# Optimization experiments

Measured on AMD Instinct MI355X. Metric: run time of the kernel, lower is better.

## Reference

```python
import jax, jax.numpy as jnp
import numpy as np

B, N, D = 16, 128, 128
NEG = jnp.float32(-9e15)
LRELU_SLOPE = 0.2
HOMO_EDGES = [1, 2, 3, 4]
HETE_EDGES = [1, 5, 6, 7, 8, 9, 10]


def _mlp_proj(x, w1, b1, w2, b2):
    # Linear(D,D) -> ReLU -> Linear(D,1)
    return jax.nn.relu(x @ w1 + b1) @ w2 + b2


def setup_inputs() -> dict:
    key = jax.random.key(0)
    ks = jax.random.split(key, 16)
    s = 0.05
    return {
        "hidden": jax.random.normal(ks[0], (B, N, D), dtype=jnp.float32),
        "adj": jax.random.randint(ks[1], (B, N, N), 0, 11),
        "node_type_mask": jax.random.randint(ks[2], (B, N), 0, 4),
        "W_Q": jax.random.normal(ks[3], (4, D, D), dtype=jnp.float32) * s,
        "W_K": jax.random.normal(ks[4], (4, D, D), dtype=jnp.float32) * s,
        "W_V": jax.random.normal(ks[5], (4, D, D), dtype=jnp.float32) * s,
        "a": jax.random.normal(ks[6], (4, D), dtype=jnp.float32) * s,  # a_params, squeezed [D,1]->[D]
        "p_w1": jax.random.normal(ks[7], (D, D), dtype=jnp.float32) * s,
        "p_b1": jnp.zeros((D,), jnp.float32),
        "p_w2": jax.random.normal(ks[8], (D, 1), dtype=jnp.float32) * s,
        "p_b2": jnp.zeros((1,), jnp.float32),
        "g_w1": jax.random.normal(ks[9], (D, D), dtype=jnp.float32) * s,
        "g_b1": jnp.zeros((D,), jnp.float32),
        "g_w2": jax.random.normal(ks[10], (D, 1), dtype=jnp.float32) * s,
        "g_b2": jnp.zeros((1,), jnp.float32),
    }


def _forward(hidden, adj, node_type_mask, W_Q, W_K, W_V, a,
             p_w1, p_b1, p_w2, p_b2, g_w1, g_b1, g_w2, g_b2):
    b, n, d = hidden.shape
    flat = hidden.reshape(-1, d)                      # [B*N, D]
    mask = node_type_mask.reshape(-1)                 # [B*N]

    # typed Q projection; nodes of type 0 stay zero (matches source)
    qh = jnp.zeros_like(flat)
    for t in range(1, 4):
        qh = jnp.where((mask == t)[:, None], flat @ W_Q[t], qh)
    q = qh.reshape(b, n, d)
    # NOTE: source bug preserved — key/value are copies of query
    k = q
    v = q

    lrelu = lambda x: jax.nn.leaky_relu(x, LRELU_SLOPE)

    # ---- homo attention on value_hidden ----
    a_input = v[:, :, None, :] * v[:, None, :, :]     # [B,N,N,D] pairwise product
    alpha = jnp.full((b, n, n), NEG, dtype=hidden.dtype)
    for r in HOMO_EDGES:
        e = lrelu(jnp.einsum('bijd,d->bij', a_input, a[r - 1]))
        alpha = jnp.where(adj == r, e, alpha)
    homo_w = jax.nn.softmax(alpha, axis=-1)
    homo_output = homo_w @ v                          # [B,N,D]

    # ---- hete attention ----
    scross = jnp.einsum('bqd,bkd->bqk', q, k)         # [B,N,N]
    global_a = jnp.tanh(scross)
    global_output = global_a @ v
    scores = jnp.full_like(scross, NEG)
    for r in HETE_EDGES:
        scores = jnp.where(adj == r, scross, scores)
    scores = lrelu(scores)
    hete_w = jax.nn.softmax(scores, axis=-1)
    hete_output = hete_w @ v                          # [B,N,D]

    # ---- gate fusion ----
    input_h = jnp.stack([homo_output, hete_output], axis=-2)   # [B,N,2,D]
    energy = _mlp_proj(input_h, p_w1, p_b1, p_w2, p_b2)        # [B,N,2,1]
    w = jax.nn.softmax(energy[..., 0], axis=-1)
    local_output = (input_h * w[..., None]).sum(axis=-2)       # [B,N,D]

    input_h2 = jnp.stack([local_output, global_output], axis=-2)
    energy2 = _mlp_proj(input_h2, g_w1, g_b1, g_w2, g_b2)
    w2 = jax.nn.softmax(energy2[..., 0], axis=-1)
    attention_output = (input_h2 * w2[..., None]).sum(axis=-2)
    return attention_output


def reference(hidden, adj, node_type_mask, W_Q, W_K, W_V, a,
              p_w1, p_b1, p_w2, p_b2, g_w1, g_b1, g_w2, g_b2):
    return _forward(hidden, adj, node_type_mask, W_Q, W_K, W_V, a,
                    p_w1, p_b1, p_w2, p_b2, g_w1, g_b1, g_w2, g_b2)
```

## Files before the change

kernel.cpp:

```cpp
#include <hip/hip_runtime.h>
#include <math.h>

#define BB 16
#define NN 128
#define DD 128
#define NEGV (-9e15f)
#define SLOPE 0.2f

__global__ __launch_bounds__(128) void hete_qproj(
    const float* __restrict__ hidden, const int* __restrict__ mask,
    const float* __restrict__ WQ, float* __restrict__ q)
{
    const int r = blockIdx.x;
    const int d = threadIdx.x;
    __shared__ float h[DD];
    h[d] = hidden[r * DD + d];
    __syncthreads();
    const int t = mask[r];
    if (t == 0) { q[r * DD + d] = 0.f; return; }
    const float* W = WQ + t * DD * DD;
    float acc = 0.f;
#pragma unroll 8
    for (int k = 0; k < DD; ++k)
        acc = fmaf(h[k], W[k * DD + d], acc);
    q[r * DD + d] = acc;
}

__global__ __launch_bounds__(256) void hete_fused(
    const float* __restrict__ q, const int* __restrict__ adj,
    const float* __restrict__ aparam,
    const float* __restrict__ p_w1, const float* __restrict__ p_b1,
    const float* __restrict__ p_w2, const float* __restrict__ p_b2,
    const float* __restrict__ g_w1, const float* __restrict__ g_b1,
    const float* __restrict__ g_w2, const float* __restrict__ g_b2,
    float* __restrict__ out)
{
    __shared__ float qs[NN][DD];
    __shared__ float a_s[4][132];
    __shared__ float wrow[2][3][NN];
    __shared__ float red[4][8];
    __shared__ float enr[8];
    __shared__ __align__(16) float ro[4][3][132];

    const int tid  = threadIdx.x;
    const int b    = blockIdx.x >> 5;
    const int chunk= blockIdx.x & 31;
    const int eh   = tid >> 7;
    const int j    = tid & 127;
    const int wv   = tid >> 6;
    const int lane = tid & 63;

    const float* qb = q + b * NN * DD;
    for (int it = 0; it < (NN * DD) / 256; ++it) {
        int idx = it * 256 + tid;
        int jj = idx >> 7, dd = idx & 127;
        qs[jj][dd ^ (jj & 31)] = qb[idx];
    }
    for (int it = 0; it < 2; ++it) {
        int idx = it * 256 + tid;
        a_s[idx >> 7][idx & 127] = aparam[idx];
    }
    __syncthreads();

    for (int rp = 0; rp < 2; ++rp) {
        const int rL = rp * 2 + eh;
        const int ri = chunk * 4 + rL;
        const int adjv = adj[(b * NN + ri) * NN + j];
        const bool inH = (adjv >= 1 && adjv <= 4);
        const bool inT = (adjv == 1) || (adjv >= 5);
        const int  rh  = inH ? (adjv - 1) : 0;
        const int  risw = ri & 31;

        float s = 0.f, hm = 0.f;
#pragma unroll 4
        for (int d = 0; d < DD; ++d) {
            float qi = qs[ri][d ^ risw];
            float qj = qs[j][d ^ (j & 31)];
            float p  = qi * qj;
            s += p;
            hm = fmaf(p, a_s[rh][d], hm);
        }

        float gw = tanhf(s);
        float aH = inH ? (hm > 0.f ? hm : SLOPE * hm) : NEGV;
        float sT = inT ? s : NEGV;
        sT = (sT > 0.f) ? sT : SLOPE * sT;

        float mH = aH, mT = sT;
        for (int off = 32; off; off >>= 1) {
            mH = fmaxf(mH, __shfl_xor(mH, off));
            mT = fmaxf(mT, __shfl_xor(mT, off));
        }
        if (lane == 0) { red[wv][0] = mH; red[wv][1] = mT; }
        __syncthreads();
        mH = fmaxf(red[eh * 2][0], red[eh * 2 + 1][0]);
        mT = fmaxf(red[eh * 2][1], red[eh * 2 + 1][1]);
        float eHv = expf(aH - mH);
        float eTv = expf(sT - mT);
        float sumH = eHv, sumT = eTv;
        for (int off = 32; off; off >>= 1) {
            sumH += __shfl_xor(sumH, off);
            sumT += __shfl_xor(sumT, off);
        }
        __syncthreads();
        if (lane == 0) { red[wv][0] = sumH; red[wv][1] = sumT; }
        __syncthreads();
        sumH = red[eh * 2][0] + red[eh * 2 + 1][0];
        sumT = red[eh * 2][1] + red[eh * 2 + 1][1];
        wrow[eh][0][j] = eHv / sumH;
        wrow[eh][1][j] = eTv / sumT;
        wrow[eh][2][j] = gw;
        __syncthreads();

        const int d = j;
        float accH = 0.f, accT = 0.f, accG = 0.f;
#pragma unroll 4
        for (int jj = 0; jj < NN; ++jj) {
            float qv = qs[jj][d ^ (jj & 31)];
            accH = fmaf(wrow[eh][0][jj], qv, accH);
            accT = fmaf(wrow[eh][1][jj], qv, accT);
            accG = fmaf(wrow[eh][2][jj], qv, accG);
        }
        ro[rL][0][d] = accH;
        ro[rL][1][d] = accT;
        ro[rL][2][d] = accG;
        __syncthreads();
    }

    const int u = j;
    {
        float a0 = 0.f, a1 = 0.f, a2 = 0.f, a3 = 0.f;
        for (int k = 0; k < DD; k += 4) {
            float w0 = p_w1[(k + 0) * DD + u];
            float w1 = p_w1[(k + 1) * DD + u];
            float w2 = p_w1[(k + 2) * DD + u];
            float w3 = p_w1[(k + 3) * DD + u];
            const float4 x0 = *reinterpret_cast<const float4*>(&ro[eh * 2 + 0][0][k]);
            const float4 x1 = *reinterpret_cast<const float4*>(&ro[eh * 2 + 0][1][k]);
            const float4 x2 = *reinterpret_cast<const float4*>(&ro[eh * 2 + 1][0][k]);
            const float4 x3 = *reinterpret_cast<const float4*>(&ro[eh * 2 + 1][1][k]);
            a0 = fmaf(x0.x, w0, fmaf(x0.y, w1, fmaf(x0.z, w2, fmaf(x0.w, w3, a0))));
            a1 = fmaf(x1.x, w0, fmaf(x1.y, w1, fmaf(x1.z, w2, fmaf(x1.w, w3, a1))));
            a2 = fmaf(x2.x, w0, fmaf(x2.y, w1, fmaf(x2.z, w2, fmaf(x2.w, w3, a2))));
            a3 = fmaf(x3.x, w0, fmaf(x3.y, w1, fmaf(x3.z, w2, fmaf(x3.w, w3, a3))));
        }
        float pb1 = p_b1[u], pw2 = p_w2[u];
        float c0 = fmaxf(a0 + pb1, 0.f) * pw2;
        float c1 = fmaxf(a1 + pb1, 0.f) * pw2;
        float c2 = fmaxf(a2 + pb1, 0.f) * pw2;
        float c3 = fmaxf(a3 + pb1, 0.f) * pw2;
        for (int off = 32; off; off >>= 1) {
            c0 += __shfl_xor(c0, off);
            c1 += __shfl_xor(c1, off);
            c2 += __shfl_xor(c2, off);
            c3 += __shfl_xor(c3, off);
        }
        if (lane == 0) { red[wv][0] = c0; red[wv][1] = c1; red[wv][2] = c2; red[wv][3] = c3; }
    }
    __syncthreads();
    if (tid < 8) {
        int half = tid >> 2;
        enr[tid] = red[half * 2][tid & 3] + red[half * 2 + 1][tid & 3] + p_b2[0];
    }
    __syncthreads();
#pragma unroll
    for (int rr = 0; rr < 2; ++rr) {
        int rL = eh * 2 + rr;
        float e0 = enr[rL * 2], e1 = enr[rL * 2 + 1];
        float m  = fmaxf(e0, e1);
        float x0 = expf(e0 - m), x1 = expf(e1 - m);
        float inv = 1.f / (x0 + x1);
        ro[rL][0][u] = (x0 * ro[rL][0][u] + x1 * ro[rL][1][u]) * inv;
    }
    __syncthreads();

    {
        float a0 = 0.f, a1 = 0.f, a2 = 0.f, a3 = 0.f;
        for (int k = 0; k < DD; k += 4) {
            float w0 = g_w1[(k + 0) * DD + u];
            float w1 = g_w1[(k + 1) * DD + u];
            float w2 = g_w1[(k + 2) * DD + u];
            float w3 = g_w1[(k + 3) * DD + u];
            const float4 x0 = *reinterpret_cast<const float4*>(&ro[eh * 2 + 0][0][k]);
            const float4 x1 = *reinterpret_cast<const float4*>(&ro[eh * 2 + 0][2][k]);
            const float4 x2 = *reinterpret_cast<const float4*>(&ro[eh * 2 + 1][0][k]);
            const float4 x3 = *reinterpret_cast<const float4*>(&ro[eh * 2 + 1][2][k]);
            a0 = fmaf(x0.x, w0, fmaf(x0.y, w1, fmaf(x0.z, w2, fmaf(x0.w, w3, a0))));
            a1 = fmaf(x1.x, w0, fmaf(x1.y, w1, fmaf(x1.z, w2, fmaf(x1.w, w3, a1))));
            a2 = fmaf(x2.x, w0, fmaf(x2.y, w1, fmaf(x2.z, w2, fmaf(x2.w, w3, a2))));
            a3 = fmaf(x3.x, w0, fmaf(x3.y, w1, fmaf(x3.z, w2, fmaf(x3.w, w3, a3))));
        }
        float gb1 = g_b1[u], gw2 = g_w2[u];
        float c0 = fmaxf(a0 + gb1, 0.f) * gw2;
        float c1 = fmaxf(a1 + gb1, 0.f) * gw2;
        float c2 = fmaxf(a2 + gb1, 0.f) * gw2;
        float c3 = fmaxf(a3 + gb1, 0.f) * gw2;
        for (int off = 32; off; off >>= 1) {
            c0 += __shfl_xor(c0, off);
            c1 += __shfl_xor(c1, off);
            c2 += __shfl_xor(c2, off);
            c3 += __shfl_xor(c3, off);
        }
        __syncthreads();
        if (lane == 0) { red[wv][0] = c0; red[wv][1] = c1; red[wv][2] = c2; red[wv][3] = c3; }
    }
    __syncthreads();
    if (tid < 8) {
        int half = tid >> 2;
        enr[tid] = red[half * 2][tid & 3] + red[half * 2 + 1][tid & 3] + g_b2[0];
    }
    __syncthreads();
#pragma unroll
    for (int rr = 0; rr < 2; ++rr) {
        int rL = eh * 2 + rr;
        float e0 = enr[rL * 2], e1 = enr[rL * 2 + 1];
        float m  = fmaxf(e0, e1);
        float x0 = expf(e0 - m), x1 = expf(e1 - m);
        float inv = 1.f / (x0 + x1);
        float val = (x0 * ro[rL][0][u] + x1 * ro[rL][2][u]) * inv;
        out[(b * NN + chunk * 4 + rL) * DD + u] = val;
    }
}

extern "C" void kernel_launch(void* const* d_in, const int* in_sizes, int n_in,
                              void* d_out, int out_size, void* d_ws, size_t ws_size,
                              hipStream_t stream) {
    const float* hidden = (const float*)d_in[0];
    const int*   adj    = (const int*)d_in[1];
    const int*   mask   = (const int*)d_in[2];
    const float* W_Q    = (const float*)d_in[3];
    const float* aparam = (const float*)d_in[6];
    const float* p_w1   = (const float*)d_in[7];
    const float* p_b1   = (const float*)d_in[8];
    const float* p_w2   = (const float*)d_in[9];
    const float* p_b2   = (const float*)d_in[10];
    const float* g_w1   = (const float*)d_in[11];
    const float* g_b1   = (const float*)d_in[12];
    const float* g_w2   = (const float*)d_in[13];
    const float* g_b2   = (const float*)d_in[14];
    float* out = (float*)d_out;
    float* qws = (float*)d_ws;

    hete_qproj<<<BB * NN, 128, 0, stream>>>(hidden, mask, W_Q, qws);
    hete_fused<<<BB * 32, 256, 0, stream>>>(qws, adj, aparam,
                                            p_w1, p_b1, p_w2, p_b2,
                                            g_w1, g_b1, g_w2, g_b2, out);
}
```

Baseline: 120.2 us.

## Rewrite fused attention kernel with bf16 split-precision MFMA and larger row tiles

Replaces the scalar FP32 pairwise-score, homo-attention and gate-MLP loops with MFMA 16x16x32 bf16 instructions, using a hi/lo bf16 split to approximate FP32 accuracy. Each block now handles 8 rows with 512 threads, precomputes q*a for the four homo edge types, and caches adj in LDS. A separate transpose kernel prepares the gate weights for the MFMA layout. The weighted-sum stage reads V as bf16-hi only, and tanh/exp become fast approximations, which lowers precision.

```diff
diff --git a/kernel.cpp b/kernel.cpp
--- a/kernel.cpp
+++ b/kernel.cpp
@@ -6,6 +6,23 @@
 #define DD 128
 #define NEGV (-9e15f)
 #define SLOPE 0.2f
+
+typedef __attribute__((ext_vector_type(8))) short bf16x8;
+typedef __attribute__((ext_vector_type(4))) float f32x4;
+
+__device__ __forceinline__ float fast_tanh(float x) {
+    float e = __expf(2.f * x);
+    return 1.f - 2.f / (e + 1.f);
+}
+__device__ __forceinline__ float bf2f(short s) {
+    union { unsigned u; float f; } v; v.u = ((unsigned)(unsigned short)s) << 16; return v.f;
+}
+__device__ __forceinline__ short f2bf(float f) {
+    union { float f; unsigned u; } v; v.f = f;
+    unsigned r = v.u + 0x7FFF + ((v.u >> 16) & 1);
+    return (short)(r >> 16);
+}
+__device__ __forceinline__ int swz(int row, int oct) { return row * 256 + ((oct ^ (row & 7)) << 4); }
 
 __global__ __launch_bounds__(128) void hete_qproj(
     const float* __restrict__ hidden, const int* __restrict__ mask,
@@ -26,199 +43,319 @@
     q[r * DD + d] = acc;
 }
 
-__global__ __launch_bounds__(256) void hete_fused(
+__global__ __launch_bounds__(256) void transpose2(
+    const float* __restrict__ A, const float* __restrict__ B,
+    float* __restrict__ AT, float* __restrict__ BT)
+{
+    __shared__ float t[16][17];
+    const int mat = blockIdx.x >> 6, tile = blockIdx.x & 63;
+    const int tr = tile >> 3, tc = tile & 7;
+    const float* S = mat ? B : A;
+    float* D = mat ? BT : AT;
+    const int r = threadIdx.x >> 4, c = threadIdx.x & 15;
+    t[r][c] = S[(tr * 16 + r) * DD + tc * 16 + c];
+    __syncthreads();
+    D[(tc * 16 + r) * DD + tr * 16 + c] = t[c][r];
+}
+
+constexpr int QH_   = 0;
+constexpr int QL_   = 32768;
+constexpr int QCHH_ = 65536;
+constexpr int QCHL_ = 69632;
+constexpr int QA_   = 73728;
+constexpr int ADJ_  = 81920;
+constexpr int WMAT_ = 86016;
+constexpr int RO_   = 102400;
+constexpr int RED_  = 114688;
+constexpr int GRED_ = 115712;
+constexpr int ENR_  = 116224;
+constexpr int SMEM_ = 116288;
+
+#define MFMA(a, b, c) __builtin_amdgcn_mfma_f32_16x16x32_bf16((a), (b), (c), 0, 0, 0)
+
+__global__ __launch_bounds__(512) void hete_fused(
     const float* __restrict__ q, const int* __restrict__ adj,
     const float* __restrict__ aparam,
-    const float* __restrict__ p_w1, const float* __restrict__ p_b1,
-    const float* __restrict__ p_w2, const float* __restrict__ p_b2,
-    const float* __restrict__ g_w1, const float* __restrict__ g_b1,
-    const float* __restrict__ g_w2, const float* __restrict__ g_b2,
+    const float* __restrict__ w1t, const float* __restrict__ g1t,
+    const float* __restrict__ p_b1, const float* __restrict__ p_w2, const float* __restrict__ p_b2,
+    const float* __restrict__ g_b1, const float* __restrict__ g_w2, const float* __restrict__ g_b2,
     float* __restrict__ out)
 {
-    __shared__ float qs[NN][DD];
-    __shared__ float a_s[4][132];
-    __shared__ float wrow[2][3][NN];
-    __shared__ float red[4][8];
-    __shared__ float enr[8];
-    __shared__ __align__(16) float ro[4][3][132];
-
-    const int tid  = threadIdx.x;
-    const int b    = blockIdx.x >> 5;
-    const int chunk= blockIdx.x & 31;
-    const int eh   = tid >> 7;
-    const int j    = tid & 127;
-    const int wv   = tid >> 6;
-    const int lane = tid & 63;
-
+    __shared__ __align__(16) char smem[SMEM_];
+    const int tid   = threadIdx.x;
+    const int b     = blockIdx.x >> 4;
+    const int chunk = blockIdx.x & 15;
+    const int wv    = tid >> 6;
+    const int lane  = tid & 63;
+    const int l15   = lane & 15;
+    const int l4    = lane >> 4;
+    const int i7    = lane & 7;
     const float* qb = q + b * NN * DD;
-    for (int it = 0; it < (NN * DD) / 256; ++it) {
-        int idx = it * 256 + tid;
-        int jj = idx >> 7, dd = idx & 127;
-        qs[jj][dd ^ (jj & 31)] = qb[idx];
-    }
-    for (int it = 0; it < 2; ++it) {
-        int idx = it * 256 + tid;
-        a_s[idx >> 7][idx & 127] = aparam[idx];
+
+#pragma unroll
+    for (int it = 0; it < 4; ++it) {
+        int oct = it * 512 + tid;
+        int row = oct >> 4, o = oct & 15;
+        const f32x4* src = (const f32x4*)(qb + row * DD + o * 8);
+        f32x4 x0 = src[0], x1 = src[1];
+        float xs[8] = {x0.x, x0.y, x0.z, x0.w, x1.x, x1.y, x1.z, x1.w};
+        bf16x8 h, l;
+#pragma unroll
+        for (int e = 0; e < 8; ++e) { short hb = f2bf(xs[e]); h[e] = hb; l[e] = f2bf(xs[e] - bf2f(hb)); }
+        *(bf16x8*)(smem + QH_ + swz(row, o)) = h;
+        *(bf16x8*)(smem + QL_ + swz(row, o)) = l;
+    }
+    if (tid < 256) {
+        int n = tid >> 4, o = tid & 15;
+        bf16x8 h = {0,0,0,0,0,0,0,0}, l = {0,0,0,0,0,0,0,0};
+        if (n < 8) {
+            const f32x4* src = (const f32x4*)(qb + (chunk * 8 + n) * DD + o * 8);
+            f32x4 x0 = src[0], x1 = src[1];
+            float xs[8] = {x0.x, x0.y, x0.z, x0.w, x1.x, x1.y, x1.z, x1.w};
+#pragma unroll
+            for (int e = 0; e < 8; ++e) { short hb = f2bf(xs[e]); h[e] = hb; l[e] = f2bf(xs[e] - bf2f(hb)); }
+        }
+        *(bf16x8*)(smem + QCHH_ + swz(n, o)) = h;
+        *(bf16x8*)(smem + QCHL_ + swz(n, o)) = l;
+    }
+    {
+        int nr = tid >> 4, o = tid & 15;
+        int t = nr >> 3, r8 = nr & 7;
+        const f32x4* sq = (const f32x4*)(qb + (chunk * 8 + r8) * DD + o * 8);
+        const f32x4* sa = (const f32x4*)(aparam + t * DD + o * 8);
+        f32x4 q0 = sq[0], q1 = sq[1], a0 = sa[0], a1 = sa[1];
+        bf16x8 v;
+        v[0] = f2bf(q0.x * a0.x); v[1] = f2bf(q0.y * a0.y);
+        v[2] = f2bf(q0.z * a0.z); v[3] = f2bf(q0.w * a0.w);
+        v[4] = f2bf(q1.x * a1.x); v[5] = f2bf(q1.y * a1.y);
+        v[6] = f2bf(q1.z * a1.z); v[7] = f2bf(q1.w * a1.w);
+        *(bf16x8*)(smem + QA_ + swz(nr, o)) = v;
+    }
+    if (tid < 256) {
+        const int4* s = (const int4*)(adj + (b * NN + chunk * 8) * NN);
+        ((int4*)(smem + ADJ_))[tid] = s[tid];
     }
     __syncthreads();
 
-    for (int rp = 0; rp < 2; ++rp) {
-        const int rL = rp * 2 + eh;
-        const int ri = chunk * 4 + rL;
-        const int adjv = adj[(b * NN + ri) * NN + j];
-        const bool inH = (adjv >= 1 && adjv <= 4);
-        const bool inT = (adjv == 1) || (adjv >= 5);
-        const int  rh  = inH ? (adjv - 1) : 0;
-        const int  risw = ri & 31;
-
-        float s = 0.f, hm = 0.f;
+    f32x4 accS  = {0.f, 0.f, 0.f, 0.f};
+    f32x4 accH0 = {0.f, 0.f, 0.f, 0.f};
+    f32x4 accH1 = {0.f, 0.f, 0.f, 0.f};
+    {
+        const int arow = wv * 16 + l15;
+#pragma unroll
+        for (int ks = 0; ks < 4; ++ks) {
+            int o = ks * 4 + l4;
+            bf16x8 Ah = *(const bf16x8*)(smem + QH_  + swz(arow, o));
+            bf16x8 Al = *(const bf16x8*)(smem + QL_  + swz(arow, o));
+            bf16x8 Bh = *(const bf16x8*)(smem + QCHH_ + swz(l15, o));
+            bf16x8 Bl = *(const bf16x8*)(smem + QCHL_ + swz(l15, o));
+            bf16x8 Q0 = *(const bf16x8*)(smem + QA_ + swz(l15, o));
+            bf16x8 Q1 = *(const bf16x8*)(smem + QA_ + swz(16 + l15, o));
+            accS  = MFMA(Ah, Bh, accS);
+            accS  = MFMA(Ah, Bl, accS);
+            accS  = MFMA(Al, Bh, accS);
+            accH0 = MFMA(Ah, Q0, accH0);
+            accH0 = MFMA(Al, Q0, accH0);
+            accH1 = MFMA(Ah, Q1, accH1);
+            accH1 = MFMA(Al, Q1, accH1);
+        }
+    }
+
+    {
+        f32x4 pH0, pH1;
+#pragma unroll
+        for (int r = 0; r < 4; ++r) {
+            pH0[r] = __shfl_xor(accH0[r], 8);
+            pH1[r] = __shfl_xor(accH1[r], 8);
+        }
+        const bool low = (l15 < 8);
+        const int* adjl = (const int*)(smem + ADJ_);
+        float aHv[4], sTv[4], gwv[4];
+#pragma unroll
+        for (int r = 0; r < 4; ++r) {
+            int j = wv * 16 + l4 * 4 + r;
+            int adjv = adjl[i7 * NN + j];
+            float s = accS[r];
+            float hm = (adjv <= 2) ? ((adjv == 1) ? accH0[r] : pH0[r])
+                                   : ((adjv == 3) ? accH1[r] : pH1[r]);
+            bool inH = (adjv >= 1) & (adjv <= 4);
+            bool inT = (adjv == 1) | (adjv >= 5);
+            float aH = inH ? (hm > 0.f ? hm : SLOPE * hm) : NEGV;
+            float sT = inT ? s : NEGV; sT = sT > 0.f ? sT : SLOPE * sT;
+            aHv[r] = aH; sTv[r] = sT; gwv[r] = fast_tanh(s);
+        }
+        float mH = fmaxf(fmaxf(aHv[0], aHv[1]), fmaxf(aHv[2], aHv[3]));
+        float mT = fmaxf(fmaxf(sTv[0], sTv[1]), fmaxf(sTv[2], sTv[3]));
+        mH = fmaxf(mH, __shfl_xor(mH, 16)); mH = fmaxf(mH, __shfl_xor(mH, 32));
+        mT = fmaxf(mT, __shfl_xor(mT, 16)); mT = fmaxf(mT, __shfl_xor(mT, 32));
+        float* red = (float*)(smem + RED_);
+        if (low && l4 == 0) { red[(wv * 8 + l15) * 4 + 0] = mH; red[(wv * 8 + l15) * 4 + 1] = mT; }
+        __syncthreads();
+        float gmH = NEGV, gmT = NEGV;
+#pragma unroll
+        for (int w = 0; w < 8; ++w) {
+            gmH = fmaxf(gmH, red[(w * 8 + i7) * 4 + 0]);
+            gmT = fmaxf(gmT, red[(w * 8 + i7) * 4 + 1]);
+        }
+        float eH[4], eT[4], pHs = 0.f, pTs = 0.f;
+#pragma unroll
+        for (int r = 0; r < 4; ++r) {
+            eH[r] = __expf(aHv[r] - gmH); pHs += eH[r];
+            eT[r] = __expf(sTv[r] - gmT); pTs += eT[r];
+        }
+        pHs += __shfl_xor(pHs, 16); pHs += __shfl_xor(pHs, 32);
+        pTs += __shfl_xor(pTs, 16); pTs += __shfl_xor(pTs, 32);
+        if (low && l4 == 0) { red[(wv * 8 + l15) * 4 + 2] = pHs; red[(wv * 8 + l15) * 4 + 3] = pTs; }
+        __syncthreads();
+        float sH = 0.f, sT2 = 0.f;
+#pragma unroll
+        for (int w = 0; w < 8; ++w) {
+            sH  += red[(w * 8 + i7) * 4 + 2];
+            sT2 += red[(w * 8 + i7) * 4 + 3];
+        }
+        float invH = 1.f / sH, invT = 1.f / sT2;
+        if (low) {
+            float4* wm = (float4*)(smem + WMAT_);
+#pragma unroll
+            for (int r = 0; r < 4; ++r) {
+                int j = wv * 16 + l4 * 4 + r;
+                wm[l15 * NN + j] = make_float4(eH[r] * invH, eT[r] * invT, gwv[r], 0.f);
+            }
+        }
+        __syncthreads();
+    }
+
+    {
+        float a0[8] = {0,0,0,0,0,0,0,0}, a1[8] = {0,0,0,0,0,0,0,0}, a2[8] = {0,0,0,0,0,0,0,0};
+        const float4* wm = (const float4*)(smem + WMAT_) + wv * NN;
 #pragma unroll 4
-        for (int d = 0; d < DD; ++d) {
-            float qi = qs[ri][d ^ risw];
-            float qj = qs[j][d ^ (j & 31)];
-            float p  = qi * qj;
-            s += p;
-            hm = fmaf(p, a_s[rh][d], hm);
-        }
-
-        float gw = tanhf(s);
-        float aH = inH ? (hm > 0.f ? hm : SLOPE * hm) : NEGV;
-        float sT = inT ? s : NEGV;
-        sT = (sT > 0.f) ? sT : SLOPE * sT;
-
-        float mH = aH, mT = sT;
-        for (int off = 32; off; off >>= 1) {
-            mH = fmaxf(mH, __shfl_xor(mH, off));
-            mT = fmaxf(mT, __shfl_xor(mT, off));
-        }
-        if (lane == 0) { red[wv][0] = mH; red[wv][1] = mT; }
-        __syncthreads();
-        mH = fmaxf(red[eh * 2][0], red[eh * 2 + 1][0]);
-        mT = fmaxf(red[eh * 2][1], red[eh * 2 + 1][1]);
-        float eHv = expf(aH - mH);
-        float eTv = expf(sT - mT);
-        float sumH = eHv, sumT = eTv;
-        for (int off = 32; off; off >>= 1) {
-            sumH += __shfl_xor(sumH, off);
-            sumT += __shfl_xor(sumT, off);
-        }
-        __syncthreads();
-        if (lane == 0) { red[wv][0] = sumH; red[wv][1] = sumT; }
-        __syncthreads();
-        sumH = red[eh * 2][0] + red[eh * 2 + 1][0];
-        sumT = red[eh * 2][1] + red[eh * 2 + 1][1];
-        wrow[eh][0][j] = eHv / sumH;
-        wrow[eh][1][j] = eTv / sumT;
-        wrow[eh][2][j] = gw;
-        __syncthreads();
-
-        const int d = j;
-        float accH = 0.f, accT = 0.f, accG = 0.f;
-#pragma unroll 4
-        for (int jj = 0; jj < NN; ++jj) {
-            float qv = qs[jj][d ^ (jj & 31)];
-            accH = fmaf(wrow[eh][0][jj], qv, accH);
-            accT = fmaf(wrow[eh][1][jj], qv, accT);
-            accG = fmaf(wrow[eh][2][jj], qv, accG);
-        }
-        ro[rL][0][d] = accH;
-        ro[rL][1][d] = accT;
-        ro[rL][2][d] = accG;
-        __syncthreads();
-    }
-
-    const int u = j;
-    {
-        float a0 = 0.f, a1 = 0.f, a2 = 0.f, a3 = 0.f;
-        for (int k = 0; k < DD; k += 4) {
-            float w0 = p_w1[(k + 0) * DD + u];
-            float w1 = p_w1[(k + 1) * DD + u];
-            float w2 = p_w1[(k + 2) * DD + u];
-            float w3 = p_w1[(k + 3) * DD + u];
-            const float4 x0 = *reinterpret_cast<const float4*>(&ro[eh * 2 + 0][0][k]);
-            const float4 x1 = *reinterpret_cast<const float4*>(&ro[eh * 2 + 0][1][k]);
-            const float4 x2 = *reinterpret_cast<const float4*>(&ro[eh * 2 + 1][0][k]);
-            const float4 x3 = *reinterpret_cast<const float4*>(&ro[eh * 2 + 1][1][k]);
-            a0 = fmaf(x0.x, w0, fmaf(x0.y, w1, fmaf(x0.z, w2, fmaf(x0.w, w3, a0))));
-            a1 = fmaf(x1.x, w0, fmaf(x1.y, w1, fmaf(x1.z, w2, fmaf(x1.w, w3, a1))));
-            a2 = fmaf(x2.x, w0, fmaf(x2.y, w1, fmaf(x2.z, w2, fmaf(x2.w, w3, a2))));
-            a3 = fmaf(x3.x, w0, fmaf(x3.y, w1, fmaf(x3.z, w2, fmaf(x3.w, w3, a3))));
-        }
-        float pb1 = p_b1[u], pw2 = p_w2[u];
-        float c0 = fmaxf(a0 + pb1, 0.f) * pw2;
-        float c1 = fmaxf(a1 + pb1, 0.f) * pw2;
-        float c2 = fmaxf(a2 + pb1, 0.f) * pw2;
-        float c3 = fmaxf(a3 + pb1, 0.f) * pw2;
-        for (int off = 32; off; off >>= 1) {
-            c0 += __shfl_xor(c0, off);
-            c1 += __shfl_xor(c1, off);
-            c2 += __shfl_xor(c2, off);
-            c3 += __shfl_xor(c3, off);
-        }
-        if (lane == 0) { red[wv][0] = c0; red[wv][1] = c1; red[wv][2] = c2; red[wv][3] = c3; }
-    }
-    __syncthreads();
-    if (tid < 8) {
-        int half = tid >> 2;
-        enr[tid] = red[half * 2][tid & 3] + red[half * 2 + 1][tid & 3] + p_b2[0];
-    }
-    __syncthreads();
-#pragma unroll
-    for (int rr = 0; rr < 2; ++rr) {
-        int rL = eh * 2 + rr;
-        float e0 = enr[rL * 2], e1 = enr[rL * 2 + 1];
-        float m  = fmaxf(e0, e1);
-        float x0 = expf(e0 - m), x1 = expf(e1 - m);
-        float inv = 1.f / (x0 + x1);
-        ro[rL][0][u] = (x0 * ro[rL][0][u] + x1 * ro[rL][1][u]) * inv;
-    }
-    __syncthreads();
-
-    {
-        float a0 = 0.f, a1 = 0.f, a2 = 0.f, a3 = 0.f;
-        for (int k = 0; k < DD; k += 4) {
-            float w0 = g_w1[(k + 0) * DD + u];
-            float w1 = g_w1[(k + 1) * DD + u];
-            float w2 = g_w1[(k + 2) * DD + u];
-            float w3 = g_w1[(k + 3) * DD + u];
-            const float4 x0 = *reinterpret_cast<const float4*>(&ro[eh * 2 + 0][0][k]);
-            const float4 x1 = *reinterpret_cast<const float4*>(&ro[eh * 2 + 0][2][k]);
-            const float4 x2 = *reinterpret_cast<const float4*>(&ro[eh * 2 + 1][0][k]);
-            const float4 x3 = *reinterpret_cast<const float4*>(&ro[eh * 2 + 1][2][k]);
-            a0 = fmaf(x0.x, w0, fmaf(x0.y, w1, fmaf(x0.z, w2, fmaf(x0.w, w3, a0))));
-            a1 = fmaf(x1.x, w0, fmaf(x1.y, w1, fmaf(x1.z, w2, fmaf(x1.w, w3, a1))));
-            a2 = fmaf(x2.x, w0, fmaf(x2.y, w1, fmaf(x2.z, w2, fmaf(x2.w, w3, a2))));
-            a3 = fmaf(x3.x, w0, fmaf(x3.y, w1, fmaf(x3.z, w2, fmaf(x3.w, w3, a3))));
-        }
-        float gb1 = g_b1[u], gw2 = g_w2[u];
-        float c0 = fmaxf(a0 + gb1, 0.f) * gw2;
-        float c1 = fmaxf(a1 + gb1, 0.f) * gw2;
-        float c2 = fmaxf(a2 + gb1, 0.f) * gw2;
-        float c3 = fmaxf(a3 + gb1, 0.f) * gw2;
-        for (int off = 32; off; off >>= 1) {
-            c0 += __shfl_xor(c0, off);
-            c1 += __shfl_xor(c1, off);
-            c2 += __shfl_xor(c2, off);
-            c3 += __shfl_xor(c3, off);
-        }
-        __syncthreads();
-        if (lane == 0) { red[wv][0] = c0; red[wv][1] = c1; red[wv][2] = c2; red[wv][3] = c3; }
-    }
-    __syncthreads();
-    if (tid < 8) {
-        int half = tid >> 2;
-        enr[tid] = red[half * 2][tid & 3] + red[half * 2 + 1][tid & 3] + g_b2[0];
-    }
-    __syncthreads();
-#pragma unroll
-    for (int rr = 0; rr < 2; ++rr) {
-        int rL = eh * 2 + rr;
-        float e0 = enr[rL * 2], e1 = enr[rL * 2 + 1];
-        float m  = fmaxf(e0, e1);
-        float x0 = expf(e0 - m), x1 = expf(e1 - m);
-        float inv = 1.f / (x0 + x1);
-        float val = (x0 * ro[rL][0][u] + x1 * ro[rL][2][u]) * inv;
-        out[(b * NN + chunk * 4 + rL) * DD + u] = val;
+        for (int jj = 0; jj < 32; ++jj) {
+            int j = l4 * 32 + jj;
+            bf16x8 qv = *(const bf16x8*)(smem + QH_ + swz(j, l15));
+            float4 w4 = wm[j];
+#pragma unroll
+            for (int e = 0; e < 8; ++e) {
+                float qf = bf2f(qv[e]);
+                a0[e] = fmaf(w4.x, qf, a0[e]);
+                a1[e] = fmaf(w4.y, qf, a1[e]);
+                a2[e] = fmaf(w4.z, qf, a2[e]);
+            }
+        }
+#pragma unroll
+        for (int e = 0; e < 8; ++e) {
+            a0[e] += __shfl_xor(a0[e], 16); a0[e] += __shfl_xor(a0[e], 32);
+            a1[e] += __shfl_xor(a1[e], 16); a1[e] += __shfl_xor(a1[e], 32);
+            a2[e] += __shfl_xor(a2[e], 16); a2[e] += __shfl_xor(a2[e], 32);
+        }
+        if (lane < 16) {
+            float* ro = (float*)(smem + RO_);
+            f32x4 v;
+            v = (f32x4){a0[0],a0[1],a0[2],a0[3]}; *(f32x4*)(ro + (0*8+wv)*DD + lane*8)     = v;
+            v = (f32x4){a0[4],a0[5],a0[6],a0[7]}; *(f32x4*)(ro + (0*8+wv)*DD + lane*8 + 4) = v;
+            v = (f32x4){a1[0],a1[1],a1[2],a1[3]}; *(f32x4*)(ro + (1*8+wv)*DD + lane*8)     = v;
+            v = (f32x4){a1[4],a1[5],a1[6],a1[7]}; *(f32x4*)(ro + (1*8+wv)*DD + lane*8 + 4) = v;
+            v = (f32x4){a2[0],a2[1],a2[2],a2[3]}; *(f32x4*)(ro + (2*8+wv)*DD + lane*8)     = v;
+            v = (f32x4){a2[4],a2[5],a2[6],a2[7]}; *(f32x4*)(ro + (2*8+wv)*DD + lane*8 + 4) = v;
+        }
+        __syncthreads();
+    }
+
+    float* ro  = (float*)(smem + RO_);
+    float* gred = (float*)(smem + GRED_);
+    float* enr  = (float*)(smem + ENR_);
+#pragma unroll
+    for (int stage = 0; stage < 2; ++stage) {
+        const float* wt  = stage ? g1t : w1t;
+        const float* b1  = stage ? g_b1 : p_b1;
+        const float* w2  = stage ? g_w2 : p_w2;
+        const float* b2  = stage ? g_b2 : p_b2;
+#pragma unroll
+        for (int it = 0; it < 4; ++it) {
+            int oct = it * 512 + tid;
+            int row = oct >> 4, o = oct & 15;
+            const f32x4* src = (const f32x4*)(wt + row * DD + o * 8);
+            f32x4 x0 = src[0], x1 = src[1];
+            float xs[8] = {x0.x, x0.y, x0.z, x0.w, x1.x, x1.y, x1.z, x1.w};
+            bf16x8 h, l;
+#pragma unroll
+            for (int e = 0; e < 8; ++e) { short hb = f2bf(xs[e]); h[e] = hb; l[e] = f2bf(xs[e] - bf2f(hb)); }
+            *(bf16x8*)(smem + QH_ + swz(row, o)) = h;
+            *(bf16x8*)(smem + QL_ + swz(row, o)) = l;
+        }
+        if (tid < 256) {
+            int e = tid >> 4, o = tid & 15;
+            int row = e >> 1;
+            int p = (e & 1) ? (stage ? 2 : 1) : 0;
+            const float* x = ro + (p * 8 + row) * DD + o * 8;
+            f32x4 x0 = *(const f32x4*)x, x1 = *(const f32x4*)(x + 4);
+            bf16x8 v;
+            v[0]=f2bf(x0.x); v[1]=f2bf(x0.y); v[2]=f2bf(x0.z); v[3]=f2bf(x0.w);
+            v[4]=f2bf(x1.x); v[5]=f2bf(x1.y); v[6]=f2bf(x1.z); v[7]=f2bf(x1.w);
+            *(bf16x8*)(smem + QA_ + swz(e, o)) = v;
+        }
+        __syncthreads();
+        f32x4 accG = {0.f, 0.f, 0.f, 0.f};
+        const int urow = wv * 16 + l15;
+#pragma unroll
+        for (int ks = 0; ks < 4; ++ks) {
+            int o = ks * 4 + l4;
+            bf16x8 Ax = *(const bf16x8*)(smem + QA_ + swz(l15, o));
+            bf16x8 Wh = *(const bf16x8*)(smem + QH_ + swz(urow, o));
+            bf16x8 Wl = *(const bf16x8*)(smem + QL_ + swz(urow, o));
+            accG = MFMA(Ax, Wh, accG);
+            accG = MFMA(Ax, Wl, accG);
+        }
+        float b1u = b1[urow], w2u = w2[urow];
+        float pe[4];
+#pragma unroll
+        for (int r = 0; r < 4; ++r) {
+            float h = accG[r] + b1u;
+            h = h > 0.f ? h : 0.f;
+            pe[r] = h * w2u;
+        }
+#pragma unroll
+        for (int off = 1; off <= 8; off <<= 1) {
+#pragma unroll
+            for (int r = 0; r < 4; ++r) pe[r] += __shfl_xor(pe[r], off);
+        }
+        if (l15 == 0) {
+#pragma unroll
+            for (int r = 0; r < 4; ++r) gred[wv * 16 + l4 * 4 + r] = pe[r];
+        }
+        __syncthreads();
+        if (tid < 16) {
+            float s = b2[0];
+#pragma unroll
+            for (int w = 0; w < 8; ++w) s += gred[w * 16 + tid];
+            enr[tid] = s;
+        }
+        __syncthreads();
+        if (stage == 0) {
+#pragma unroll
+            for (int k = 0; k < 2; ++k) {
+                int idx = k * 512 + tid;
+                int row = idx >> 7, d = idx & 127;
+                float e0 = enr[row * 2], e1 = enr[row * 2 + 1];
+                float m = fmaxf(e0, e1);
+                float x0 = __expf(e0 - m), x1 = __expf(e1 - m);
+                float inv = 1.f / (x0 + x1);
+                ro[(0 * 8 + row) * DD + d] =
+                    (x0 * ro[(0 * 8 + row) * DD + d] + x1 * ro[(1 * 8 + row) * DD + d]) * inv;
+            }
+            __syncthreads();
+        } else {
+#pragma unroll
+            for (int k = 0; k < 2; ++k) {
+                int idx = k * 512 + tid;
+                int row = idx >> 7, d = idx & 127;
+                float e0 = enr[row * 2], e1 = enr[row * 2 + 1];
+                float m = fmaxf(e0, e1);
+                float x0 = __expf(e0 - m), x1 = __expf(e1 - m);
+                float inv = 1.f / (x0 + x1);
+                float val = (x0 * ro[(0 * 8 + row) * DD + d] + x1 * ro[(2 * 8 + row) * DD + d]) * inv;
+                out[(b * NN + chunk * 8 + row) * DD + d] = val;
+            }
+        }
     }
 }
 
@@ -226,8 +363,8 @@
                               void* d_out, int out_size, void* d_ws, size_t ws_size,
                               hipStream_t stream) {
     const float* hidden = (const float*)d_in[0];
-    const int*   adj    = (const int*)d_in[1];
-    const int*   mask   = (const int*)d_in[2];
+    const int*   adjp   = (const int*)d_in[1];
+    const int*   maskp  = (const int*)d_in[2];
     const float* W_Q    = (const float*)d_in[3];
     const float* aparam = (const float*)d_in[6];
     const float* p_w1   = (const float*)d_in[7];
@@ -239,10 +376,13 @@
     const float* g_w2   = (const float*)d_in[13];
     const float* g_b2   = (const float*)d_in[14];
     float* out = (float*)d_out;
+
     float* qws = (float*)d_ws;
-
-    hete_qproj<<<BB * NN, 128, 0, stream>>>(hidden, mask, W_Q, qws);
-    hete_fused<<<BB * 32, 256, 0, stream>>>(qws, adj, aparam,
-                                            p_w1, p_b1, p_w2, p_b2,
-                                            g_w1, g_b1, g_w2, g_b2, out);
-}
+    float* w1t = (float*)((char*)d_ws + (1u << 20));
+    float* g1t = (float*)((char*)d_ws + (1u << 20) + 65536);
+
+    hete_qproj<<<BB * NN, 128, 0, stream>>>(hidden, maskp, W_Q, qws);
+    transpose2<<<128, 256, 0, stream>>>(p_w1, g_w1, w1t, g1t);
+    hete_fused<<<BB * 16, 512, 0, stream>>>(qws, adjp, aparam, w1t, g1t,
+                                            p_b1, p_w2, p_b2, g_b1, g_w2, g_b2, out);
+}
```

Measured after the change: 106.3 us. 11.6% less time.
